# Kernel tuning notes

Measured on AMD Instinct MI355X. Metric: run time of the kernel, lower is better.

## Reference

```python
import jax, jax.numpy as jnp
import numpy as np

C = 256
CQK = C // 8  # query/key channels from Conv2d(in_dim, in_dim//8, 1)


def _cross_attn(x, y, qw, qb, kw, kb, vw, vb, gamma):
    # x, y: [B, C, H, W]; 1x1 convs are channel matmuls
    B, Cc, H, W = x.shape
    N = H * W
    xf = x.reshape(B, Cc, N)
    yf = y.reshape(B, Cc, N)
    q = jnp.einsum('oc,bcn->bno', qw, xf) + qb  # [B, N, CQK]
    k = jnp.einsum('oc,bcn->bon', kw, yf) + kb[:, None]  # [B, CQK, N]
    energy = jnp.einsum('bnc,bcm->bnm', q, k)  # [B, N, N]
    attn = jax.nn.softmax(energy, axis=2)
    v = jnp.einsum('oc,bcn->bon', vw, yf) + vb[:, None]  # [B, C, N]
    out = jnp.einsum('bcm,bnm->bcn', v, attn)  # value @ attention^T
    out = out.reshape(B, Cc, H, W)
    return gamma * out + x


def setup_inputs() -> dict:
    key = jax.random.key(0)
    ks = jax.random.split(key, 16)
    B, H, W = 4, 64, 64
    s = 1.0 / np.sqrt(C)
    d = {
        'x': jax.random.normal(ks[0], (B, C, H, W), jnp.float32),
        'y': jax.random.normal(ks[1], (B, C, H, W), jnp.float32),
        'z': jax.random.normal(ks[2], (B, C, H, W), jnp.float32),
        'q1_w': jax.random.normal(ks[3], (CQK, C), jnp.float32) * s,
        'q1_b': jax.random.normal(ks[4], (CQK,), jnp.float32) * s,
        'k1_w': jax.random.normal(ks[5], (CQK, C), jnp.float32) * s,
        'k1_b': jax.random.normal(ks[6], (CQK,), jnp.float32) * s,
        'v1_w': jax.random.normal(ks[7], (C, C), jnp.float32) * s,
        'v1_b': jax.random.normal(ks[8], (C,), jnp.float32) * s,
        'gamma1': jax.random.normal(ks[9], (1,), jnp.float32) * 0.1,
        'q2_w': jax.random.normal(ks[10], (CQK, C), jnp.float32) * s,
        'q2_b': jax.random.normal(ks[11], (CQK,), jnp.float32) * s,
        'k2_w': jax.random.normal(ks[12], (CQK, C), jnp.float32) * s,
        'k2_b': jax.random.normal(ks[13], (CQK,), jnp.float32) * s,
        'v2_w': jax.random.normal(ks[14], (C, C), jnp.float32) * s,
        'v2_b': jax.random.normal(ks[15], (C,), jnp.float32) * s,
        'gamma2': jax.random.normal(jax.random.fold_in(key, 99), (1,), jnp.float32) * 0.1,
    }
    return d


def reference(x, y, z, q1_w, q1_b, k1_w, k1_b, v1_w, v1_b, gamma1,
              q2_w, q2_b, k2_w, k2_b, v2_w, v2_b, gamma2):
    out1 = _cross_attn(x, y, q1_w, q1_b, k1_w, k1_b, v1_w, v1_b, gamma1)
    out2 = _cross_attn(out1, z, q2_w, q2_b, k2_w, k2_b, v2_w, v2_b, gamma2)
    return out2
```

## Files before the change

kernel.cpp:

```cpp
#include <hip/hip_runtime.h>
#include <hip/hip_bf16.h>

#define NSEQ 4096
#define CDIM 256
#define CQKD 32
#define LOG2E 1.4426950408889634f

typedef float v4f __attribute__((ext_vector_type(4)));
typedef float v16f __attribute__((ext_vector_type(16)));
typedef short v8s __attribute__((ext_vector_type(8)));
typedef unsigned long long u64;

__device__ __forceinline__ float exp2_(float x) {
#if __has_builtin(__builtin_amdgcn_exp2f)
  return __builtin_amdgcn_exp2f(x);
#else
  float r;
  __asm__("v_exp_f32 %0, %1" : "=v"(r) : "v"(x));
  return r;
#endif
}

__device__ __forceinline__ unsigned short f2bf(float x) {
  unsigned u = __builtin_bit_cast(unsigned, x);
  unsigned r = (u + 0x7FFFu + ((u >> 16) & 1u)) >> 16;
  return (unsigned short)r;
}
__device__ __forceinline__ float bf2f(unsigned short s) {
  unsigned u = ((unsigned)s) << 16;
  return __builtin_bit_cast(float, u);
}
__device__ __forceinline__ unsigned int pack_bf16(float a, float b) {
#if __has_builtin(__builtin_amdgcn_cvt_pk_bf16_f32)
  typedef __bf16 v2bf __attribute__((ext_vector_type(2)));
  v2bf r = __builtin_amdgcn_cvt_pk_bf16_f32(a, b);
  return __builtin_bit_cast(unsigned int, r);
#else
  return ((unsigned)f2bf(b) << 16) | (unsigned)f2bf(a);
#endif
}

__device__ __forceinline__ unsigned char f2e4m3(float x) {
  unsigned u = __builtin_bit_cast(unsigned, x);
  unsigned s = (u >> 24) & 0x80u;
  unsigned au = u & 0x7fffffffu;
  if (au > 0x43e00000u) return (unsigned char)(s | 0x7eu);
  if (au < 0x3c800000u) {
    float ax = __builtin_bit_cast(float, au);
    int q = (int)(ax * 512.0f + 0.5f);
    if (q > 7) q = 7;
    return (unsigned char)(s | (unsigned)q);
  }
  int e = (int)((au >> 23) & 0xffu) - 127 + 7;
  unsigned m = au & 0x7fffffu;
  unsigned mr = m + 0x7ffffu + ((m >> 20) & 1u);
  if (mr >= 0x800000u) { mr -= 0x800000u; e += 1; if (e >= 16) return (unsigned char)(s | 0x7e); }
  return (unsigned char)(s | ((unsigned)e << 3) | (mr >> 20));
}
__device__ __forceinline__ unsigned int pack4_fp8(float a, float b, float c, float d) {
#if __has_builtin(__builtin_amdgcn_cvt_pk_fp8_f32)
  int v = 0;
  v = __builtin_amdgcn_cvt_pk_fp8_f32(a, b, v, false);
  v = __builtin_amdgcn_cvt_pk_fp8_f32(c, d, v, true);
  return (unsigned int)v;
#else
  return (unsigned)f2e4m3(a) | ((unsigned)f2e4m3(b) << 8) |
         ((unsigned)f2e4m3(c) << 16) | ((unsigned)f2e4m3(d) << 24);
#endif
}

__device__ __forceinline__ void barrier_lds() {
  __asm__ __volatile__("s_waitcnt lgkmcnt(0)\n\ts_barrier" ::: "memory");
}

__global__ __launch_bounds__(256) void convw_kernel(
    const float* __restrict__ q1w, const float* __restrict__ k1w,
    const float* __restrict__ k2w, const float* __restrict__ q2w,
    const float* __restrict__ v1w, const float* __restrict__ v2w,
    unsigned short* __restrict__ W) {
  const int s = blockIdx.x * 256 + threadIdx.x;
  const float* src;
  int o, ch0;
  size_t obase;
  float scale = 1.0f;
  if (s < 3072) {
    const int wsel = s >> 10, r = s & 1023;
    src = wsel == 0 ? q1w : (wsel == 1 ? k1w : k2w);
    const int ot = r >> 9, cb = (r >> 6) & 7, lane = r & 63;
    o = ot * 16 + (lane & 15);
    ch0 = cb * 32 + ((lane >> 4) & 3) * 8;
    obase = (size_t)wsel * 8192 + (size_t)r * 8;
  } else if (s < 19456) {
    const int s2 = s - 3072, which = s2 >> 13, r = s2 & 8191;
    src = which == 0 ? v1w : v2w;
    const int ot = r >> 9, cb = (r >> 6) & 7, lane = r & 63;
    o = ot * 16 + (lane & 15);
    ch0 = cb * 32 + ((lane >> 4) & 3) * 8;
    obase = 32768 + (size_t)which * 65536 + (size_t)r * 8;
  } else {
    const int r = s - 19456;
    src = q2w;
    const int lane = r & 63;
    o = lane & 31;
    ch0 = (r >> 6) * 16 + (lane >> 5) * 8;
    obase = 24576 + (size_t)r * 8;
    scale = LOG2E;
  }
#pragma unroll
  for (int j = 0; j < 8; ++j)
    W[obase + j] = f2bf(src[o * CDIM + ch0 + j] * scale);
}

__global__ __launch_bounds__(256) void prep_kernel(
    const float* __restrict__ x, const float* __restrict__ y,
    const float* __restrict__ z, const unsigned short* __restrict__ Wbf,
    const float* __restrict__ q1b, const float* __restrict__ k1b,
    const float* __restrict__ k2b, const float* __restrict__ v1b,
    const float* __restrict__ v2b, unsigned short* __restrict__ Q1,
    unsigned short* __restrict__ K1, unsigned short* __restrict__ K2,
    unsigned char* __restrict__ V1, unsigned char* __restrict__ V2) {
  __shared__ unsigned short t[256][72];
  __shared__ unsigned short Kt[64][40];
  const int src = blockIdx.z;
  const float* in = src == 0 ? x : (src == 1 ? y : z);
  const int b = blockIdx.y;
  const int n0 = blockIdx.x * 64;
  const int tid = threadIdx.x, lane = tid & 63, w = tid >> 6;
  const int quad = lane >> 4, r15 = lane & 15, l31 = lane & 31, lh = lane >> 5;
  const float* ip = in + (size_t)(b * CDIM) * NSEQ + n0;
  {
    const int chb = tid >> 4, c4 = (tid & 15) * 4;
#pragma unroll
    for (int p = 0; p < 16; ++p) {
      const int ch = p * 16 + chb;
      float4 v = *(const float4*)(ip + (size_t)ch * NSEQ + c4);
      uint2 pk;
      pk.x = pack_bf16(v.x, v.y);
      pk.y = pack_bf16(v.z, v.w);
      *(uint2*)&t[ch][c4] = pk;
    }
  }
  __syncthreads();
  v8s af[8];
#pragma unroll
  for (int cb = 0; cb < 8; ++cb) {
    union { unsigned short e[8]; v8s v; } u;
#pragma unroll
    for (int j = 0; j < 8; ++j) u.e[j] = t[cb * 32 + quad * 8 + j][w * 16 + r15];
    af[cb] = u.v;
  }
  const int nt = blockIdx.x * 4 + w;
  const unsigned short* Wqk = Wbf + src * 8192;
  v4f a0 = {0.f, 0.f, 0.f, 0.f}, a1 = a0;
#pragma unroll
  for (int cb = 0; cb < 8; ++cb) {
    v8s b0 = *(const v8s*)(Wqk + (size_t)cb * 512 + lane * 8);
    v8s b1 = *(const v8s*)(Wqk + (size_t)(8 + cb) * 512 + lane * 8);
    a0 = __builtin_amdgcn_mfma_f32_16x16x32_bf16(af[cb], b0, a0, 0, 0, 0);
    a1 = __builtin_amdgcn_mfma_f32_16x16x32_bf16(af[cb], b1, a1, 0, 0, 0);
  }
  if (src == 0) {
#pragma unroll
    for (int r = 0; r < 4; ++r) {
      Q1[((size_t)b * NSEQ + nt * 16 + quad * 4 + r) * CQKD + r15] =
          f2bf((a0[r] + q1b[r15]) * LOG2E);
      Q1[((size_t)b * NSEQ + nt * 16 + quad * 4 + r) * CQKD + 16 + r15] =
          f2bf((a1[r] + q1b[16 + r15]) * LOG2E);
    }
    return;
  }
  const float* kbias = src == 1 ? k1b : k2b;
#pragma unroll
  for (int r = 0; r < 4; ++r) {
    Kt[w * 16 + quad * 4 + r][r15] = f2bf(a0[r] + kbias[r15]);
    Kt[w * 16 + quad * 4 + r][16 + r15] = f2bf(a1[r] + kbias[16 + r15]);
  }
  const unsigned short* Wv = Wbf + 32768 + (src - 1) * 65536;
  const float* vbias = src == 1 ? v1b : v2b;
  v4f vacc[16];
#pragma unroll
  for (int ot = 0; ot < 16; ++ot) vacc[ot] = (v4f){0.f, 0.f, 0.f, 0.f};
#pragma unroll
  for (int cb = 0; cb < 8; ++cb) {
    const v8s afc = af[cb];
#pragma unroll
    for (int ot = 0; ot < 16; ++ot) {
      v8s bf = *(const v8s*)(Wv + (size_t)(ot * 8 + cb) * 512 + lane * 8);
      vacc[ot] = __builtin_amdgcn_mfma_f32_16x16x32_bf16(afc, bf, vacc[ot], 0, 0, 0);
    }
  }
  __syncthreads();
  unsigned char* Vt8 = (unsigned char*)t;
#pragma unroll
  for (int ot = 0; ot < 16; ++ot) {
    const int ch = ot * 16 + r15;
    const float bv = vbias[ch];
    *(unsigned int*)&Vt8[(size_t)ch * 72 + w * 16 + quad * 4] =
        pack4_fp8(vacc[ot][0] + bv, vacc[ot][1] + bv, vacc[ot][2] + bv, vacc[ot][3] + bv);
  }
  {
    unsigned short* Kout = (src == 1 ? K1 : K2) + (size_t)b * (NSEQ / 16) * 512;
    *(v8s*)(Kout + ((size_t)nt * 64 + lane) * 8) = *(const v8s*)&Kt[w * 16 + r15][quad * 8];
  }
  __syncthreads();
  unsigned char* Vout = (src == 1 ? V1 : V2) + (size_t)b * (NSEQ / 16) * 8 * 512;
#pragma unroll
  for (int chb = 0; chb < 8; ++chb)
    *(u64*)(Vout + (((size_t)nt * 8 + chb) * 64 + lane) * 8) =
        *(const u64*)&Vt8[(size_t)(chb * 32 + l31) * 72 + w * 16 + lh * 8];
}


__device__ __forceinline__ void max_pass16(
    const unsigned short* __restrict__ Kp, const v8s qf[4], int w, int lane,
    float (*lbuf)[64], float m[4]) {
  const v4f vzero4 = {0.f, 0.f, 0.f, 0.f};
  const int r15 = lane & 15;
  const unsigned short* Kl = Kp + (size_t)w * 512 + lane * 8;
  v8s kA = *(const v8s*)(Kl);
  v8s kB = *(const v8s*)(Kl + 8192);
#pragma unroll
  for (int qt = 0; qt < 4; ++qt) m[qt] = -3.0e38f;
#pragma unroll 2
  for (int kt = 0; kt < 16; ++kt) {
    v8s kC = *(const v8s*)(Kl + (size_t)((kt + 2) & 15) * 8192);
#pragma unroll
    for (int qt = 0; qt < 4; ++qt) {
      v4f st = __builtin_amdgcn_mfma_f32_16x16x32_bf16(kA, qf[qt], vzero4, 0, 0, 0);
      m[qt] = fmaxf(m[qt], fmaxf(fmaxf(st[0], st[1]), fmaxf(st[2], st[3])));
    }
    kA = kB;
    kB = kC;
  }
#pragma unroll
  for (int qt = 0; qt < 4; ++qt) {
    m[qt] = fmaxf(m[qt], __shfl_xor(m[qt], 16));
    m[qt] = fmaxf(m[qt], __shfl_xor(m[qt], 32));
  }
  if (lane < 16) {
#pragma unroll
    for (int qt = 0; qt < 4; ++qt) lbuf[w][qt * 16 + lane] = m[qt];
  }
  __syncthreads();
#pragma unroll
  for (int qt = 0; qt < 4; ++qt) {
    float mm = lbuf[0][qt * 16 + r15];
#pragma unroll
    for (int ww = 1; ww < 16; ++ww) mm = fmaxf(mm, lbuf[ww][qt * 16 + r15]);
    m[qt] = mm;
  }
  __syncthreads();
}

__device__ __forceinline__ void s_phase(
    unsigned char* __restrict__ P, int pbuf, const v8s kf, const v8s qf[4],
    const float m[4], int w, int lane, float lsum[4]) {
  const v4f vzero4 = {0.f, 0.f, 0.f, 0.f};
  const int quad = lane >> 4, r15 = lane & 15;
  unsigned char* pw = P + pbuf * 8704 + w * 16 + quad * 4;
#pragma unroll
  for (int qt = 0; qt < 4; ++qt) {
    v4f st = __builtin_amdgcn_mfma_f32_16x16x32_bf16(kf, qf[qt], vzero4, 0, 0, 0);
    float e0 = exp2_(st[0] - m[qt]), e1 = exp2_(st[1] - m[qt]);
    float e2 = exp2_(st[2] - m[qt]), e3 = exp2_(st[3] - m[qt]);
    lsum[qt] += (e0 + e1) + (e2 + e3);
    *(unsigned int*)(pw + (size_t)(qt * 16 + r15) * 136) = pack4_fp8(e0, e1, e2, e3);
  }
}

__device__ __forceinline__ void pv_tile(
    const unsigned char* __restrict__ P, int pbuf, const u64 vf[8], int lane,
    v16f acc[2]) {
  const int l31 = lane & 31, lh = lane >> 5;
  const unsigned char* pb = P + pbuf * 8704;
  __builtin_amdgcn_s_setprio(1);
#pragma unroll
  for (int s = 0; s < 8; ++s) {
    long pf0 = (long)*(const u64*)(pb + (size_t)l31 * 136 + s * 16 + lh * 8);
    long pf1 = (long)*(const u64*)(pb + (size_t)(32 + l31) * 136 + s * 16 + lh * 8);
    acc[0] = __builtin_amdgcn_mfma_f32_32x32x16_fp8_fp8((long)vf[s], pf0, acc[0], 0, 0, 0);
    acc[1] = __builtin_amdgcn_mfma_f32_32x32x16_fp8_fp8((long)vf[s], pf1, acc[1], 0, 0, 0);
  }
  __builtin_amdgcn_s_setprio(0);
}

__device__ __forceinline__ void attn_loop(
    const unsigned short* __restrict__ Kp, const unsigned char* __restrict__ Vp,
    unsigned char* __restrict__ P, const v8s qf[4], const float m[4], int w, int lane,
    v16f acc[2], float lsum[4]) {
  if (w < 8) {
    const unsigned short* Kl = Kp + (size_t)w * 512 + lane * 8;
    v8s k0 = *(const v8s*)(Kl);
    v8s k1 = *(const v8s*)(Kl + 4096);
    s_phase(P, 0, k0, qf, m, w, lane, lsum);
    k0 = *(const v8s*)(Kl + 2 * 4096);
    s_phase(P, 1, k1, qf, m, w, lane, lsum);
    k1 = *(const v8s*)(Kl + 3 * 4096);
    barrier_lds();
#pragma unroll 1
    for (int p = 1; p < 16; ++p) {
      const int bs = (p & 1) * 2;
      s_phase(P, bs, k0, qf, m, w, lane, lsum);
      k0 = *(const v8s*)(Kl + (size_t)((2 * p + 2) & 31) * 4096);
      s_phase(P, bs + 1, k1, qf, m, w, lane, lsum);
      k1 = *(const v8s*)(Kl + (size_t)((2 * p + 3) & 31) * 4096);
      barrier_lds();
    }
    barrier_lds();
  } else {
    const unsigned char* Vl = Vp + (size_t)(w - 8) * 512 + lane * 8;
    u64 v0[8], v1[8];
#pragma unroll
    for (int s = 0; s < 8; ++s) v0[s] = *(const u64*)(Vl + (size_t)s * 4096);
#pragma unroll
    for (int s = 0; s < 8; ++s) v1[s] = *(const u64*)(Vl + 32768 + (size_t)s * 4096);
    barrier_lds();
#pragma unroll 1
    for (int p = 0; p < 15; ++p) {
      const int bs = (p & 1) * 2;
      pv_tile(P, bs, v0, lane, acc);
#pragma unroll
      for (int s = 0; s < 8; ++s)
        v0[s] = *(const u64*)(Vl + (size_t)(2 * p + 2) * 32768 + s * 4096);
      pv_tile(P, bs + 1, v1, lane, acc);
#pragma unroll
      for (int s = 0; s < 8; ++s)
        v1[s] = *(const u64*)(Vl + (size_t)(2 * p + 3) * 32768 + s * 4096);
      barrier_lds();
    }
    pv_tile(P, 2, v0, lane, acc);
    pv_tile(P, 3, v1, lane, acc);
    barrier_lds();
  }
}

__global__ __launch_bounds__(1024, 4) void fused_attn_kernel(
    const unsigned short* __restrict__ Q1g, const unsigned short* __restrict__ K1g,
    const unsigned char* __restrict__ V1g, const unsigned short* __restrict__ K2g,
    const unsigned char* __restrict__ V2g, const unsigned short* __restrict__ W2g,
    const float* __restrict__ x, const float* __restrict__ q2b,
    const float* __restrict__ g1p, const float* __restrict__ g2p,
    float* __restrict__ outp) {
  __shared__ __align__(16) unsigned char P[4 * 8704];
  __shared__ __align__(16) unsigned short out1T[64 * 264];
  __shared__ __align__(16) unsigned short q2s[64 * 32];
  __shared__ float lbuf[16][64];

  const int tid = threadIdx.x;
  const int lane = tid & 63;
  const int w = tid >> 6;
  const int quad = lane >> 4;
  const int r15 = lane & 15;
  const int l31 = lane & 31, lh = lane >> 5;
  const int b = blockIdx.x & 3;
  const int n0 = (blockIdx.x >> 2) * 64;

  const float g1 = g1p[0];
  const float g2 = g2p[0];

  const unsigned short* Qp  = Q1g + (size_t)b * NSEQ * CQKD;
  const unsigned short* K1p = K1g + (size_t)b * (NSEQ / 16) * 512;
  const unsigned short* K2p = K2g + (size_t)b * (NSEQ / 16) * 512;
  const unsigned char* V1p  = V1g + (size_t)b * (NSEQ / 16) * 8 * 512;
  const unsigned char* V2p  = V2g + (size_t)b * (NSEQ / 16) * 8 * 512;

  v8s qf[4];
#pragma unroll
  for (int qt = 0; qt < 4; ++qt)
    qf[qt] = *(const v8s*)(Qp + (n0 + qt * 16 + r15) * CQKD + quad * 8);

  v16f acc[2];
  float lsum[4] = {0.f, 0.f, 0.f, 0.f};
  float m[4];
  acc[0] = (v16f)(0.f); acc[1] = (v16f)(0.f);

  max_pass16(K1p, qf, w, lane, lbuf, m);
  attn_loop(K1p, V1p, P, qf, m, w, lane, acc, lsum);
  if (w < 8) {
#pragma unroll
    for (int qt = 0; qt < 4; ++qt) {
      lsum[qt] += __shfl_xor(lsum[qt], 16);
      lsum[qt] += __shfl_xor(lsum[qt], 32);
    }
    if (lane < 16) {
#pragma unroll
      for (int qt = 0; qt < 4; ++qt) lbuf[w][qt * 16 + lane] = lsum[qt];
    }
  }
  __syncthreads();
  float rinv[2];
#pragma unroll
  for (int qh = 0; qh < 2; ++qh) {
    const int q = qh * 32 + l31;
    float d = 0.f;
#pragma unroll
    for (int ww = 0; ww < 8; ++ww) d += lbuf[ww][q];
    rinv[qh] = 1.0f / d;
  }
  if (w >= 8) {
    const int cw = (w - 8) * 32;
#pragma unroll
    for (int qh = 0; qh < 2; ++qh) {
      const int q = qh * 32 + l31;
#pragma unroll
      for (int rg = 0; rg < 4; ++rg) {
        const int c = cw + 8 * rg + 4 * lh;
        float o0 = g1 * (acc[qh][rg * 4 + 0] * rinv[qh]) + x[((size_t)b * CDIM + c + 0) * NSEQ + n0 + q];
        float o1 = g1 * (acc[qh][rg * 4 + 1] * rinv[qh]) + x[((size_t)b * CDIM + c + 1) * NSEQ + n0 + q];
        float o2 = g1 * (acc[qh][rg * 4 + 2] * rinv[qh]) + x[((size_t)b * CDIM + c + 2) * NSEQ + n0 + q];
        float o3 = g1 * (acc[qh][rg * 4 + 3] * rinv[qh]) + x[((size_t)b * CDIM + c + 3) * NSEQ + n0 + q];
        uint2 pk;
        pk.x = pack_bf16(o0, o1);
        pk.y = pack_bf16(o2, o3);
        *(uint2*)(out1T + (size_t)q * 264 + c) = pk;
      }
    }
  }
  __syncthreads();

  if (w < 2) {
    const int qh = w;
    v16f qacc = (v16f)(0.f);
#pragma unroll
    for (int s = 0; s < 16; ++s) {
      v8s af = *(const v8s*)(W2g + (size_t)(s * 64 + lane) * 8);
      v8s bf = *(const v8s*)(out1T + (size_t)(qh * 32 + l31) * 264 + s * 16 + lh * 8);
      qacc = __builtin_amdgcn_mfma_f32_32x32x16_bf16(af, bf, qacc, 0, 0, 0);
    }
#pragma unroll
    for (int rg = 0; rg < 4; ++rg) {
      const int o = 8 * rg + 4 * lh;
      uint2 pk;
      pk.x = pack_bf16(qacc[rg * 4 + 0] + q2b[o + 0] * LOG2E, qacc[rg * 4 + 1] + q2b[o + 1] * LOG2E);
      pk.y = pack_bf16(qacc[rg * 4 + 2] + q2b[o + 2] * LOG2E, qacc[rg * 4 + 3] + q2b[o + 3] * LOG2E);
      *(uint2*)(q2s + (size_t)(qh * 32 + l31) * 32 + o) = pk;
    }
  }
  __syncthreads();

#pragma unroll
  for (int qt = 0; qt < 4; ++qt)
    qf[qt] = *(const v8s*)(q2s + (qt * 16 + r15) * 32 + quad * 8);
  acc[0] = (v16f)(0.f); acc[1] = (v16f)(0.f);
#pragma unroll
  for (int qt = 0; qt < 4; ++qt) lsum[qt] = 0.f;
  max_pass16(K2p, qf, w, lane, lbuf, m);
  attn_loop(K2p, V2p, P, qf, m, w, lane, acc, lsum);
  if (w < 8) {
#pragma unroll
    for (int qt = 0; qt < 4; ++qt) {
      lsum[qt] += __shfl_xor(lsum[qt], 16);
      lsum[qt] += __shfl_xor(lsum[qt], 32);
    }
    if (lane < 16) {
#pragma unroll
      for (int qt = 0; qt < 4; ++qt) lbuf[w][qt * 16 + lane] = lsum[qt];
    }
  }
  __syncthreads();
#pragma unroll
  for (int qh = 0; qh < 2; ++qh) {
    const int q = qh * 32 + l31;
    float d = 0.f;
#pragma unroll
    for (int ww = 0; ww < 8; ++ww) d += lbuf[ww][q];
    rinv[qh] = 1.0f / d;
  }
  if (w >= 8) {
    const int cw = (w - 8) * 32;
#pragma unroll
    for (int qh = 0; qh < 2; ++qh) {
      const int q = qh * 32 + l31;
#pragma unroll
      for (int rg = 0; rg < 4; ++rg) {
        const int c = cw + 8 * rg + 4 * lh;
#pragma unroll
        for (int i = 0; i < 4; ++i) {
          float res = bf2f(out1T[(size_t)q * 264 + c + i]);
          outp[((size_t)b * CDIM + c + i) * NSEQ + n0 + q] =
              g2 * (acc[qh][rg * 4 + i] * rinv[qh]) + res;
        }
      }
    }
  }
}

extern "C" void kernel_launch(void* const* d_in, const int* in_sizes, int n_in,
                              void* d_out, int out_size, void* d_ws, size_t ws_size,
                              hipStream_t stream) {
  const float* x   = (const float*)d_in[0];
  const float* y   = (const float*)d_in[1];
  const float* z   = (const float*)d_in[2];
  const float* q1w = (const float*)d_in[3];
  const float* q1b = (const float*)d_in[4];
  const float* k1w = (const float*)d_in[5];
  const float* k1b = (const float*)d_in[6];
  const float* v1w = (const float*)d_in[7];
  const float* v1b = (const float*)d_in[8];
  const float* g1  = (const float*)d_in[9];
  const float* q2w = (const float*)d_in[10];
  const float* q2b = (const float*)d_in[11];
  const float* k2w = (const float*)d_in[12];
  const float* k2b = (const float*)d_in[13];
  const float* v2w = (const float*)d_in[14];
  const float* v2b = (const float*)d_in[15];
  const float* g2  = (const float*)d_in[16];
  char* ws = (char*)d_ws;
  unsigned short* Wbf = (unsigned short*)(ws);
  unsigned short* Q1  = (unsigned short*)(ws + 327680);
  unsigned short* K1  = (unsigned short*)(ws + 1376256);
  unsigned short* K2  = (unsigned short*)(ws + 2424832);
  unsigned char*  V1  = (unsigned char*)(ws + 3473408);
  unsigned char*  V2  = (unsigned char*)(ws + 7667712);
  float* outp = (float*)d_out;

  convw_kernel<<<dim3(80), 256, 0, stream>>>(q1w, k1w, k2w, q2w, v1w, v2w, Wbf);
  prep_kernel<<<dim3(64, 4, 3), 256, 0, stream>>>(x, y, z, Wbf, q1b, k1b, k2b, v1b,
                                                  v2b, Q1, K1, K2, V1, V2);
  fused_attn_kernel<<<dim3(256), 1024, 0, stream>>>(Q1, K1, V1, K2, V2, Wbf + 24576, x,
                                                    q2b, g1, g2, outp);
}
```

Before: 210.3 us.

## Replace block barriers with LDS counter producer-consumer ring between softmax and PV waves

Replaces the per-iteration workgroup barriers between the score/softmax waves and the PV waves with per-slot LDS atomic counters, using a four-slot ring of P buffers (doubling P shared memory). Producers poll a consumer counter before overwriting a slot and signal after writing; consumers poll the producer counter and signal after reading. This is meant to decouple the two wave groups so neither stalls on a full-block barrier, at the cost of more LDS use (possibly lower occupancy), spin-polling overhead, and relaxed-ordering correctness risks.

```diff
diff --git a/kernel.cpp b/kernel.cpp
--- a/kernel.cpp
+++ b/kernel.cpp
@@ -67,10 +67,6 @@
   return (unsigned)f2e4m3(a) | ((unsigned)f2e4m3(b) << 8) |
          ((unsigned)f2e4m3(c) << 16) | ((unsigned)f2e4m3(d) << 24);
 #endif
-}
-
-__device__ __forceinline__ void barrier_lds() {
-  __asm__ __volatile__("s_waitcnt lgkmcnt(0)\n\ts_barrier" ::: "memory");
 }
 
 __global__ __launch_bounds__(256) void convw_kernel(
@@ -211,6 +207,22 @@
 }
 
 
+__device__ __forceinline__ void poll_ge(const unsigned* p, unsigned target) {
+  for (int i = 0; i < (1 << 20); ++i) {
+    unsigned v = __hip_atomic_load(p, __ATOMIC_RELAXED, __HIP_MEMORY_SCOPE_WORKGROUP);
+    if (v >= target) break;
+    __builtin_amdgcn_s_sleep(1);
+  }
+  __builtin_amdgcn_sched_barrier(0);
+  __asm__ __volatile__("" ::: "memory");
+}
+__device__ __forceinline__ void signal_cnt(unsigned* p, int lane) {
+  __asm__ __volatile__("s_waitcnt lgkmcnt(0)" ::: "memory");
+  __builtin_amdgcn_sched_barrier(0);
+  if (lane == 0)
+    __hip_atomic_fetch_add(p, 1u, __ATOMIC_RELAXED, __HIP_MEMORY_SCOPE_WORKGROUP);
+}
+
 __device__ __forceinline__ void max_pass16(
     const unsigned short* __restrict__ Kp, const v8s qf[4], int w, int lane,
     float (*lbuf)[64], float m[4]) {
@@ -286,27 +298,26 @@
 
 __device__ __forceinline__ void attn_loop(
     const unsigned short* __restrict__ Kp, const unsigned char* __restrict__ Vp,
-    unsigned char* __restrict__ P, const v8s qf[4], const float m[4], int w, int lane,
-    v16f acc[2], float lsum[4]) {
+    unsigned char* __restrict__ P, unsigned* __restrict__ prod_cnt,
+    unsigned* __restrict__ cons_cnt, const v8s qf[4], const float m[4], int w,
+    int lane, v16f acc[2], float lsum[4]) {
   if (w < 8) {
     const unsigned short* Kl = Kp + (size_t)w * 512 + lane * 8;
     v8s k0 = *(const v8s*)(Kl);
     v8s k1 = *(const v8s*)(Kl + 4096);
-    s_phase(P, 0, k0, qf, m, w, lane, lsum);
-    k0 = *(const v8s*)(Kl + 2 * 4096);
-    s_phase(P, 1, k1, qf, m, w, lane, lsum);
-    k1 = *(const v8s*)(Kl + 3 * 4096);
-    barrier_lds();
 #pragma unroll 1
-    for (int p = 1; p < 16; ++p) {
-      const int bs = (p & 1) * 2;
-      s_phase(P, bs, k0, qf, m, w, lane, lsum);
-      k0 = *(const v8s*)(Kl + (size_t)((2 * p + 2) & 31) * 4096);
-      s_phase(P, bs + 1, k1, qf, m, w, lane, lsum);
-      k1 = *(const v8s*)(Kl + (size_t)((2 * p + 3) & 31) * 4096);
-      barrier_lds();
-    }
-    barrier_lds();
+    for (int p = 0; p < 16; ++p) {
+      const int slot = p & 3;
+      const unsigned it = (unsigned)(p >> 2);
+      v8s kn0 = *(const v8s*)(Kl + (size_t)((2 * p + 2) & 31) * 4096);
+      v8s kn1 = *(const v8s*)(Kl + (size_t)((2 * p + 3) & 31) * 4096);
+      poll_ge(&cons_cnt[slot], 8u * it);
+      s_phase(P, 2 * slot, k0, qf, m, w, lane, lsum);
+      s_phase(P, 2 * slot + 1, k1, qf, m, w, lane, lsum);
+      signal_cnt(&prod_cnt[slot], lane);
+      k0 = kn0;
+      k1 = kn1;
+    }
   } else {
     const unsigned char* Vl = Vp + (size_t)(w - 8) * 512 + lane * 8;
     u64 v0[8], v1[8];
@@ -314,23 +325,21 @@
     for (int s = 0; s < 8; ++s) v0[s] = *(const u64*)(Vl + (size_t)s * 4096);
 #pragma unroll
     for (int s = 0; s < 8; ++s) v1[s] = *(const u64*)(Vl + 32768 + (size_t)s * 4096);
-    barrier_lds();
 #pragma unroll 1
-    for (int p = 0; p < 15; ++p) {
-      const int bs = (p & 1) * 2;
-      pv_tile(P, bs, v0, lane, acc);
+    for (int p = 0; p < 16; ++p) {
+      const int slot = p & 3;
+      const unsigned it = (unsigned)(p >> 2);
+      poll_ge(&prod_cnt[slot], 8u * (it + 1));
+      pv_tile(P, 2 * slot, v0, lane, acc);
 #pragma unroll
       for (int s = 0; s < 8; ++s)
-        v0[s] = *(const u64*)(Vl + (size_t)(2 * p + 2) * 32768 + s * 4096);
-      pv_tile(P, bs + 1, v1, lane, acc);
+        v0[s] = *(const u64*)(Vl + (size_t)((2 * p + 2) & 31) * 32768 + s * 4096);
+      pv_tile(P, 2 * slot + 1, v1, lane, acc);
 #pragma unroll
       for (int s = 0; s < 8; ++s)
-        v1[s] = *(const u64*)(Vl + (size_t)(2 * p + 3) * 32768 + s * 4096);
-      barrier_lds();
-    }
-    pv_tile(P, 2, v0, lane, acc);
-    pv_tile(P, 3, v1, lane, acc);
-    barrier_lds();
+        v1[s] = *(const u64*)(Vl + (size_t)((2 * p + 3) & 31) * 32768 + s * 4096);
+      signal_cnt(&cons_cnt[slot], lane);
+    }
   }
 }
 
@@ -341,10 +350,11 @@
     const float* __restrict__ x, const float* __restrict__ q2b,
     const float* __restrict__ g1p, const float* __restrict__ g2p,
     float* __restrict__ outp) {
-  __shared__ __align__(16) unsigned char P[4 * 8704];
+  __shared__ __align__(16) unsigned char P[8 * 8704];
   __shared__ __align__(16) unsigned short out1T[64 * 264];
   __shared__ __align__(16) unsigned short q2s[64 * 32];
   __shared__ float lbuf[16][64];
+  __shared__ unsigned prod_cnt[4], cons_cnt[4];
 
   const int tid = threadIdx.x;
   const int lane = tid & 63;
@@ -374,8 +384,9 @@
   float m[4];
   acc[0] = (v16f)(0.f); acc[1] = (v16f)(0.f);
 
+  if (tid < 4) { prod_cnt[tid] = 0; cons_cnt[tid] = 0; }
   max_pass16(K1p, qf, w, lane, lbuf, m);
-  attn_loop(K1p, V1p, P, qf, m, w, lane, acc, lsum);
+  attn_loop(K1p, V1p, P, prod_cnt, cons_cnt, qf, m, w, lane, acc, lsum);
   if (w < 8) {
 #pragma unroll
     for (int qt = 0; qt < 4; ++qt) {
@@ -444,8 +455,9 @@
   acc[0] = (v16f)(0.f); acc[1] = (v16f)(0.f);
 #pragma unroll
   for (int qt = 0; qt < 4; ++qt) lsum[qt] = 0.f;
+  if (tid < 4) { prod_cnt[tid] = 0; cons_cnt[tid] = 0; }
   max_pass16(K2p, qf, w, lane, lbuf, m);
-  attn_loop(K2p, V2p, P, qf, m, w, lane, acc, lsum);
+  attn_loop(K2p, V2p, P, prod_cnt, cons_cnt, qf, m, w, lane, acc, lsum);
   if (w < 8) {
 #pragma unroll
     for (int qt = 0; qt < 4; ++qt) {
```

Result: no change. 207.2 us (-1.4%).
